# Optimization experiments

Hardware: AMD Instinct MI355X
Metric: run time of the kernel (lower is better)

## Reference

```python
import jax, jax.numpy as jnp
import numpy as np

GRID_SHAPE = (64, 64, 64)  # final-stage density grid
N_STAGE = 3                # len(proj_channels)


def _stage_projection(stage, pos, node_features, origin, lattice, batch_nodes, Wp, bp, scale):
    """pairwise_similarity + project_onto_grid for one stage.
    pos: (B, N, 3) padded positions; node_features: (B, N, E) padded.
    Returns (B, C, nx, ny, nz).
    """
    B, N, _ = pos.shape
    down = 2 ** (N_STAGE - stage - 1)
    n_xyz = tuple(s // down for s in GRID_SHAPE)
    l = jnp.diagonal(lattice[0])  # (3,) lattice lengths (uses first batch entry, as original)
    axes = [jnp.linspace(0.0, l[i], n_xyz[i]) for i in range(3)]
    grid = jnp.stack(jnp.meshgrid(*axes, indexing='ij'), axis=-1).reshape(1, -1, 3)
    grid = grid + origin[:, None, :]                       # (B, G, 3)
    # cdist^2 via |a|^2 + |b|^2 - 2 a.b (avoids (B,G,N,3) diff tensor)
    g2 = jnp.sum(grid * grid, axis=-1)                     # (B, G)
    p2 = jnp.sum(pos * pos, axis=-1)                       # (B, N)
    d2 = g2[:, :, None] + p2[:, None, :] - 2.0 * jnp.einsum('bgd,bnd->bgn', grid, pos)
    d2 = jnp.maximum(d2, 0.0)                              # (B, G, N)
    s = scale[stage]
    lorentz = s / (s * s + d2)                             # Lorentzian kernel
    # padded nodes: distance was set to inf -> weight 0
    valid = jnp.arange(N)[None, :] < batch_nodes[:, None]  # (B, N)
    w = jnp.where(valid[:, None, :], lorentz, 0.0)         # (B, G, N)
    nf = node_features @ Wp[stage] + bp[stage]             # (B, N, C)
    x = jnp.einsum('bgn,bnc->bgc', w, nf)                  # node -> grid reduction
    C = nf.shape[-1]
    x = x.transpose(0, 2, 1).reshape(B, C, *n_xyz)
    return x


def setup_inputs() -> dict:
    key = jax.random.key(0)
    ks = jax.random.split(key, 8)
    B, N, E, C = 8, 64, 128, 32
    pos = jax.random.uniform(ks[0], (B, N, 3), dtype=jnp.float32) * 10.0
    node_features = jax.random.normal(ks[1], (B, N, E), dtype=jnp.float32)
    origin = jax.random.normal(ks[2], (B, 3), dtype=jnp.float32)
    lattice = jnp.tile(jnp.diag(jnp.array([12.0, 12.0, 12.0], dtype=jnp.float32))[None], (B, 1, 1))
    batch_nodes = jax.random.randint(ks[3], (B,), 32, N + 1)
    Wp = jax.random.normal(ks[4], (N_STAGE, E, C), dtype=jnp.float32) * 0.05
    bp = jax.random.normal(ks[5], (N_STAGE, C), dtype=jnp.float32) * 0.01
    scale = 0.5 + 0.2 * (jax.random.uniform(ks[6], (N_STAGE,), dtype=jnp.float32) - 0.5)
    return {"pos": pos, "node_features": node_features, "origin": origin,
            "lattice": lattice, "batch_nodes": batch_nodes,
            "Wp": Wp, "bp": bp, "scale": scale}


def reference(pos, node_features, origin, lattice, batch_nodes, Wp, bp, scale):
    B = pos.shape[0]
    x = None
    for stage in range(N_STAGE):
        x_grid = _stage_projection(stage, pos, node_features, origin, lattice,
                                   batch_nodes, Wp, bp, scale)
        if stage == 0:
            x = x_grid
        else:
            # trilinear upsample, half-pixel centers == torch align_corners=False
            x = jax.image.resize(x, x_grid.shape, method='trilinear')
            x = x + x_grid
    return x
```

## Files before the change

### kernel.cpp

```cpp
#include <hip/hip_runtime.h>


constexpr int NB = 8;
constexpr int NNODE = 64;
constexpr int NE = 128;
constexpr int NC = 32;

__global__ void nf_kernel(const float* __restrict__ node_features,
                          const float* __restrict__ Wp,
                          const float* __restrict__ bp,
                          const float* __restrict__ scale,
                          float* __restrict__ nf)
{
    int idx = blockIdx.x * 256 + threadIdx.x;
    int c = idx & (NC - 1);
    int n = (idx >> 5) & (NNODE - 1);
    int b = (idx >> 11) & (NB - 1);
    int s = idx >> 14;
    const float* f = node_features + (b * NNODE + n) * NE;
    const float* w = Wp + s * NE * NC + c;
    float acc = bp[s * NC + c];
#pragma unroll 8
    for (int e = 0; e < NE; ++e)
        acc = fmaf(f[e], w[e * NC], acc);
    nf[idx] = acc * scale[s];
}

template <int STAGE, int NX>
__global__ __launch_bounds__(256) void stage_kernel(
        const float* __restrict__ pos,
        const float* __restrict__ origin,
        const float* __restrict__ lattice,
        const int*   __restrict__ batch_nodes,
        const float* __restrict__ scale,
        const float* __restrict__ nf,
        const float* __restrict__ prev,
        float* __restrict__ outp)
{
    constexpr int LOG = (NX == 16) ? 4 : (NX == 32) ? 5 : 6;
    constexpr int G = NX * NX * NX;
    constexpr int TPB = G / 256;

    __shared__ float4 nfs[NNODE][NC / 4];
    __shared__ float4 poss[NNODE];

    const int b = blockIdx.x / TPB;
    const int g = (blockIdx.x % TPB) * 256 + threadIdx.x;

    const float* __restrict__ nrow = nf + (STAGE * NB + b) * NNODE * NC;
    {
        const float4* n4 = reinterpret_cast<const float4*>(nrow);
        int t = threadIdx.x;
        nfs[t >> 3][t & 7] = n4[t];
        t += 256;
        nfs[t >> 3][t & 7] = n4[t];
        if (threadIdx.x < NNODE) {
            const float* p = pos + (b * NNODE + threadIdx.x) * 3;
            float px = p[0], py = p[1], pz = p[2];
            poss[threadIdx.x] = make_float4(-2.0f * px, -2.0f * py, -2.0f * pz,
                                            fmaf(px, px, fmaf(py, py, pz * pz)));
        }
    }

    const int iz = g & (NX - 1);
    const int iy = (g >> LOG) & (NX - 1);
    const int ix = g >> (2 * LOG);

    const float stx = lattice[0] / (float)(NX - 1);
    const float sty = lattice[4] / (float)(NX - 1);
    const float stz = lattice[8] / (float)(NX - 1);
    const float gx = fmaf((float)ix, stx, origin[b * 3 + 0]);
    const float gy = fmaf((float)iy, sty, origin[b * 3 + 1]);
    const float gz = fmaf((float)iz, stz, origin[b * 3 + 2]);

    const float s  = scale[STAGE];
    const float s2 = s * s;
    const float g2s2 = fmaf(gx, gx, fmaf(gy, gy, fmaf(gz, gz, s2)));
    const int nn = batch_nodes[b];

    float acc[NC];
#pragma unroll
    for (int c = 0; c < NC; ++c) acc[c] = 0.0f;

    __syncthreads();

#pragma unroll 2
    for (int n = 0; n < nn; ++n) {
        const float4 pq = poss[n];
        float t = fmaf(pq.x, gx, pq.w);
        t = fmaf(pq.y, gy, t);
        t = fmaf(pq.z, gz, t);
        const float denom = fmaxf(t + g2s2, s2);
        const float w = __builtin_amdgcn_rcpf(denom);
#pragma unroll
        for (int c4 = 0; c4 < NC / 4; ++c4) {
            const float4 v = nfs[n][c4];
            acc[c4 * 4 + 0] = fmaf(w, v.x, acc[c4 * 4 + 0]);
            acc[c4 * 4 + 1] = fmaf(w, v.y, acc[c4 * 4 + 1]);
            acc[c4 * 4 + 2] = fmaf(w, v.z, acc[c4 * 4 + 2]);
            acc[c4 * 4 + 3] = fmaf(w, v.w, acc[c4 * 4 + 3]);
        }
    }

    float* __restrict__ o = outp + (size_t)(b * NC) * G + g;

    if constexpr (STAGE == 0) {
#pragma unroll
        for (int c = 0; c < NC; ++c) o[(size_t)c * G] = acc[c];
    } else {
        constexpr int NH = NX / 2;
        constexpr int GH = NH * NH * NH;
        int x0i = (ix >> 1) - 1 + (ix & 1); int x1i = x0i + 1;
        int y0i = (iy >> 1) - 1 + (iy & 1); int y1i = y0i + 1;
        int z0i = (iz >> 1) - 1 + (iz & 1); int z1i = z0i + 1;
        const float wxl = (ix & 1) ? 0.75f : 0.25f;
        const float wyl = (iy & 1) ? 0.75f : 0.25f;
        const float wzl = (iz & 1) ? 0.75f : 0.25f;
        if (x0i < 0) x0i = 0; if (x1i > NH - 1) x1i = NH - 1;
        if (y0i < 0) y0i = 0; if (y1i > NH - 1) y1i = NH - 1;
        if (z0i < 0) z0i = 0; if (z1i > NH - 1) z1i = NH - 1;
        const float wxh = 1.0f - wxl, wyh = 1.0f - wyl, wzh = 1.0f - wzl;

        const int o000 = (x0i * NH + y0i) * NH + z0i;
        const int o001 = (x0i * NH + y0i) * NH + z1i;
        const int o010 = (x0i * NH + y1i) * NH + z0i;
        const int o011 = (x0i * NH + y1i) * NH + z1i;
        const int o100 = (x1i * NH + y0i) * NH + z0i;
        const int o101 = (x1i * NH + y0i) * NH + z1i;
        const int o110 = (x1i * NH + y1i) * NH + z0i;
        const int o111 = (x1i * NH + y1i) * NH + z1i;

        const float w000 = wxl * wyl * wzl, w001 = wxl * wyl * wzh;
        const float w010 = wxl * wyh * wzl, w011 = wxl * wyh * wzh;
        const float w100 = wxh * wyl * wzl, w101 = wxh * wyl * wzh;
        const float w110 = wxh * wyh * wzl, w111 = wxh * wyh * wzh;

        const float* __restrict__ pb = prev + (size_t)(b * NC) * GH;
#pragma unroll
        for (int c = 0; c < NC; ++c) {
            const float* __restrict__ pc = pb + (size_t)c * GH;
            float up = w000 * pc[o000] + w001 * pc[o001]
                     + w010 * pc[o010] + w011 * pc[o011]
                     + w100 * pc[o100] + w101 * pc[o101]
                     + w110 * pc[o110] + w111 * pc[o111];
            float r = up + acc[c];
            if constexpr (STAGE == 2)
                __builtin_nontemporal_store(r, &o[(size_t)c * G]);
            else
                o[(size_t)c * G] = r;
        }
    }
}

extern "C" void kernel_launch(void* const* d_in, const int* in_sizes, int n_in,
                              void* d_out, int out_size, void* d_ws, size_t ws_size,
                              hipStream_t stream) {
    const float* pos           = (const float*)d_in[0];
    const float* node_features = (const float*)d_in[1];
    const float* origin        = (const float*)d_in[2];
    const float* lattice       = (const float*)d_in[3];
    const int*   batch_nodes   = (const int*)d_in[4];
    const float* Wp            = (const float*)d_in[5];
    const float* bp            = (const float*)d_in[6];
    const float* scale         = (const float*)d_in[7];
    float* out = (float*)d_out;

    float* wsf = (float*)d_ws;
    float* nf = wsf;
    float* x0 = wsf + 49152;
    float* x1 = x0 + (size_t)NB * NC * 16 * 16 * 16;

    nf_kernel<<<dim3(192), dim3(256), 0, stream>>>(node_features, Wp, bp, scale, nf);

    stage_kernel<0, 16><<<dim3(NB * 16), dim3(256), 0, stream>>>(
        pos, origin, lattice, batch_nodes, scale, nf, (const float*)nullptr, x0);

    stage_kernel<1, 32><<<dim3(NB * 128), dim3(256), 0, stream>>>(
        pos, origin, lattice, batch_nodes, scale, nf, x0, x1);

    stage_kernel<2, 64><<<dim3(NB * 1024), dim3(256), 0, stream>>>(
        pos, origin, lattice, batch_nodes, scale, nf, x1, out);
}
```

Before: 542.3 us.

## Compute four z-adjacent grid points per thread with vectorized stores and shared upsample taps

```diff
diff --git a/kernel.cpp b/kernel.cpp
--- a/kernel.cpp
+++ b/kernel.cpp
@@ -5,6 +5,9 @@
 constexpr int NNODE = 64;
 constexpr int NE = 128;
 constexpr int NC = 32;
+constexpr int KG = 4;
+
+typedef float f32x4 __attribute__((ext_vector_type(4)));
 
 __global__ void nf_kernel(const float* __restrict__ node_features,
                           const float* __restrict__ Wp,
@@ -27,7 +30,7 @@
 }
 
 template <int STAGE, int NX>
-__global__ __launch_bounds__(256) void stage_kernel(
+__global__ __launch_bounds__(256, 3) void stage_kernel(
         const float* __restrict__ pos,
         const float* __restrict__ origin,
         const float* __restrict__ lattice,
@@ -39,13 +42,17 @@
 {
     constexpr int LOG = (NX == 16) ? 4 : (NX == 32) ? 5 : 6;
     constexpr int G = NX * NX * NX;
-    constexpr int TPB = G / 256;
+    constexpr int NZB = NX / KG;
 
     __shared__ float4 nfs[NNODE][NC / 4];
     __shared__ float4 poss[NNODE];
 
-    const int b = blockIdx.x / TPB;
-    const int g = (blockIdx.x % TPB) * 256 + threadIdx.x;
+    const int gid = blockIdx.x * 256 + threadIdx.x;
+    const int b = gid >> (3 * LOG - 2);
+    const int izb = gid & (NZB - 1);
+    const int iy = (gid >> (LOG - 2)) & (NX - 1);
+    const int ix = (gid >> (2 * LOG - 2)) & (NX - 1);
+    const int iz0 = izb * KG;
 
     const float* __restrict__ nrow = nf + (STAGE * NB + b) * NNODE * NC;
     {
@@ -62,92 +69,108 @@
         }
     }
 
-    const int iz = g & (NX - 1);
-    const int iy = (g >> LOG) & (NX - 1);
-    const int ix = g >> (2 * LOG);
-
     const float stx = lattice[0] / (float)(NX - 1);
     const float sty = lattice[4] / (float)(NX - 1);
     const float stz = lattice[8] / (float)(NX - 1);
     const float gx = fmaf((float)ix, stx, origin[b * 3 + 0]);
     const float gy = fmaf((float)iy, sty, origin[b * 3 + 1]);
-    const float gz = fmaf((float)iz, stz, origin[b * 3 + 2]);
-
     const float s  = scale[STAGE];
     const float s2 = s * s;
-    const float g2s2 = fmaf(gx, gx, fmaf(gy, gy, fmaf(gz, gz, s2)));
+    const float gxy2 = fmaf(gx, gx, fmaf(gy, gy, s2));
+
+    float gz[KG], g2s2[KG];
+#pragma unroll
+    for (int j = 0; j < KG; ++j) {
+        gz[j] = fmaf((float)(iz0 + j), stz, origin[b * 3 + 2]);
+        g2s2[j] = fmaf(gz[j], gz[j], gxy2);
+    }
+
     const int nn = batch_nodes[b];
 
-    float acc[NC];
-#pragma unroll
-    for (int c = 0; c < NC; ++c) acc[c] = 0.0f;
+    float acc[KG][NC];
+#pragma unroll
+    for (int j = 0; j < KG; ++j)
+#pragma unroll
+        for (int c = 0; c < NC; ++c) acc[j][c] = 0.0f;
 
     __syncthreads();
 
 #pragma unroll 2
     for (int n = 0; n < nn; ++n) {
         const float4 pq = poss[n];
-        float t = fmaf(pq.x, gx, pq.w);
-        t = fmaf(pq.y, gy, t);
-        t = fmaf(pq.z, gz, t);
-        const float denom = fmaxf(t + g2s2, s2);
-        const float w = __builtin_amdgcn_rcpf(denom);
+        const float txy = fmaf(pq.x, gx, fmaf(pq.y, gy, pq.w));
+        float w[KG];
+#pragma unroll
+        for (int j = 0; j < KG; ++j) {
+            const float t = fmaf(pq.z, gz[j], txy);
+            w[j] = __builtin_amdgcn_rcpf(fmaxf(t + g2s2[j], s2));
+        }
 #pragma unroll
         for (int c4 = 0; c4 < NC / 4; ++c4) {
             const float4 v = nfs[n][c4];
-            acc[c4 * 4 + 0] = fmaf(w, v.x, acc[c4 * 4 + 0]);
-            acc[c4 * 4 + 1] = fmaf(w, v.y, acc[c4 * 4 + 1]);
-            acc[c4 * 4 + 2] = fmaf(w, v.z, acc[c4 * 4 + 2]);
-            acc[c4 * 4 + 3] = fmaf(w, v.w, acc[c4 * 4 + 3]);
-        }
-    }
-
-    float* __restrict__ o = outp + (size_t)(b * NC) * G + g;
+#pragma unroll
+            for (int j = 0; j < KG; ++j) {
+                acc[j][c4 * 4 + 0] = fmaf(w[j], v.x, acc[j][c4 * 4 + 0]);
+                acc[j][c4 * 4 + 1] = fmaf(w[j], v.y, acc[j][c4 * 4 + 1]);
+                acc[j][c4 * 4 + 2] = fmaf(w[j], v.z, acc[j][c4 * 4 + 2]);
+                acc[j][c4 * 4 + 3] = fmaf(w[j], v.w, acc[j][c4 * 4 + 3]);
+            }
+        }
+    }
+
+    float* __restrict__ o = outp + (size_t)(b * NC) * G + ((ix << LOG) + iy) * NX + iz0;
 
     if constexpr (STAGE == 0) {
 #pragma unroll
-        for (int c = 0; c < NC; ++c) o[(size_t)c * G] = acc[c];
+        for (int c = 0; c < NC; ++c) {
+            float4 r = make_float4(acc[0][c], acc[1][c], acc[2][c], acc[3][c]);
+            *reinterpret_cast<float4*>(&o[(size_t)c * G]) = r;
+        }
     } else {
         constexpr int NH = NX / 2;
         constexpr int GH = NH * NH * NH;
         int x0i = (ix >> 1) - 1 + (ix & 1); int x1i = x0i + 1;
         int y0i = (iy >> 1) - 1 + (iy & 1); int y1i = y0i + 1;
-        int z0i = (iz >> 1) - 1 + (iz & 1); int z1i = z0i + 1;
         const float wxl = (ix & 1) ? 0.75f : 0.25f;
         const float wyl = (iy & 1) ? 0.75f : 0.25f;
-        const float wzl = (iz & 1) ? 0.75f : 0.25f;
         if (x0i < 0) x0i = 0; if (x1i > NH - 1) x1i = NH - 1;
         if (y0i < 0) y0i = 0; if (y1i > NH - 1) y1i = NH - 1;
-        if (z0i < 0) z0i = 0; if (z1i > NH - 1) z1i = NH - 1;
-        const float wxh = 1.0f - wxl, wyh = 1.0f - wyl, wzh = 1.0f - wzl;
-
-        const int o000 = (x0i * NH + y0i) * NH + z0i;
-        const int o001 = (x0i * NH + y0i) * NH + z1i;
-        const int o010 = (x0i * NH + y1i) * NH + z0i;
-        const int o011 = (x0i * NH + y1i) * NH + z1i;
-        const int o100 = (x1i * NH + y0i) * NH + z0i;
-        const int o101 = (x1i * NH + y0i) * NH + z1i;
-        const int o110 = (x1i * NH + y1i) * NH + z0i;
-        const int o111 = (x1i * NH + y1i) * NH + z1i;
-
-        const float w000 = wxl * wyl * wzl, w001 = wxl * wyl * wzh;
-        const float w010 = wxl * wyh * wzl, w011 = wxl * wyh * wzh;
-        const float w100 = wxh * wyl * wzl, w101 = wxh * wyl * wzh;
-        const float w110 = wxh * wyh * wzl, w111 = wxh * wyh * wzh;
+        const float wxh = 1.0f - wxl, wyh = 1.0f - wyl;
+        const float w00 = wxl * wyl, w01 = wxl * wyh;
+        const float w10 = wxh * wyl, w11 = wxh * wyh;
+
+        const int k2 = iz0 >> 1;
+        int zs[4];
+        zs[0] = k2 - 1 < 0 ? 0 : k2 - 1;
+        zs[1] = k2;
+        zs[2] = k2 + 1;
+        zs[3] = k2 + 2 > NH - 1 ? NH - 1 : k2 + 2;
+
+        const int r00 = (x0i * NH + y0i) * NH;
+        const int r01 = (x0i * NH + y1i) * NH;
+        const int r10 = (x1i * NH + y0i) * NH;
+        const int r11 = (x1i * NH + y1i) * NH;
 
         const float* __restrict__ pb = prev + (size_t)(b * NC) * GH;
 #pragma unroll
         for (int c = 0; c < NC; ++c) {
             const float* __restrict__ pc = pb + (size_t)c * GH;
-            float up = w000 * pc[o000] + w001 * pc[o001]
-                     + w010 * pc[o010] + w011 * pc[o011]
-                     + w100 * pc[o100] + w101 * pc[o101]
-                     + w110 * pc[o110] + w111 * pc[o111];
-            float r = up + acc[c];
+            float v[4];
+#pragma unroll
+            for (int zi = 0; zi < 4; ++zi) {
+                const int z = zs[zi];
+                v[zi] = w00 * pc[r00 + z] + w01 * pc[r01 + z]
+                      + w10 * pc[r10 + z] + w11 * pc[r11 + z];
+            }
+            f32x4 r;
+            r.x = fmaf(0.25f, v[0], fmaf(0.75f, v[1], acc[0][c]));
+            r.y = fmaf(0.75f, v[1], fmaf(0.25f, v[2], acc[1][c]));
+            r.z = fmaf(0.25f, v[1], fmaf(0.75f, v[2], acc[2][c]));
+            r.w = fmaf(0.75f, v[2], fmaf(0.25f, v[3], acc[3][c]));
             if constexpr (STAGE == 2)
-                __builtin_nontemporal_store(r, &o[(size_t)c * G]);
+                __builtin_nontemporal_store(r, reinterpret_cast<f32x4*>(&o[(size_t)c * G]));
             else
-                o[(size_t)c * G] = r;
+                *reinterpret_cast<f32x4*>(&o[(size_t)c * G]) = r;
         }
     }
 }
@@ -172,12 +195,12 @@
 
     nf_kernel<<<dim3(192), dim3(256), 0, stream>>>(node_features, Wp, bp, scale, nf);
 
-    stage_kernel<0, 16><<<dim3(NB * 16), dim3(256), 0, stream>>>(
+    stage_kernel<0, 16><<<dim3(NB * 4096 / KG / 256), dim3(256), 0, stream>>>(
         pos, origin, lattice, batch_nodes, scale, nf, (const float*)nullptr, x0);
 
-    stage_kernel<1, 32><<<dim3(NB * 128), dim3(256), 0, stream>>>(
+    stage_kernel<1, 32><<<dim3(NB * 32768 / KG / 256), dim3(256), 0, stream>>>(
         pos, origin, lattice, batch_nodes, scale, nf, x0, x1);
 
-    stage_kernel<2, 64><<<dim3(NB * 1024), dim3(256), 0, stream>>>(
+    stage_kernel<2, 64><<<dim3(NB * 262144 / KG / 256), dim3(256), 0, stream>>>(
         pos, origin, lattice, batch_nodes, scale, nf, x1, out);
 }
```

New measurement: 479.0 us. 1.13x faster.
